# Optimization experiments

Hardware: AMD Instinct MI355X
Metric: run time of the kernel (lower is better)

## Reference

```python
import jax, jax.numpy as jnp
import numpy as np

B, T, C = 2, 2048, 1024
H = 16
D = C // H  # head_dim = 64
EPS = 1e-06
MAX_SEQ = 2048


def make_rotary(dim, max_seq_len, base=10000):
    inv_freq = 1.0 / (base ** (jnp.arange(0, dim, 2, dtype=jnp.float32) / dim))
    pos = jnp.arange(max_seq_len, dtype=jnp.float32)
    sinusoid = jnp.einsum('i,j->ij', pos, inv_freq)  # (S, dim//2)
    return jnp.sin(sinusoid), jnp.cos(sinusoid)


def apply_rotary(x, sin, cos):
    # x: (B, T, H, D); sin/cos: (MAX_SEQ, D//2)
    t = x.shape[1]
    s = sin[:t][:, None, :]  # (T,1,D//2) broadcasts over B and H
    c = cos[:t][:, None, :]
    d = x.shape[-1]
    x1, x2 = x[..., :d // 2], x[..., d // 2:]
    return jnp.concatenate([x1 * c - x2 * s, x2 * c + x1 * s], axis=-1)


def yat_dense(x, kernel, bias, alpha, eps=EPS):
    # Yat layer: squared dot product over squared euclidean distance.
    dot = x @ kernel                                   # (..., out)
    x_sq = jnp.sum(x * x, axis=-1, keepdims=True)      # (..., 1)
    k_sq = jnp.sum(kernel * kernel, axis=0)            # (out,)
    dist = x_sq + k_sq - 2.0 * dot
    y = (dot * dot) / (dist + eps)
    out_f = kernel.shape[1]
    scale = (jnp.sqrt(jnp.float32(out_f)) / jnp.log(1.0 + jnp.float32(out_f))) ** alpha
    return y * scale + bias


def setup_inputs() -> dict:
    key = jax.random.key(0)
    ks = jax.random.split(key, 7)
    x = jax.random.normal(ks[0], (B, T, C), dtype=jnp.float32)
    mask = jnp.tril(jnp.ones((T, T), dtype=bool))[None].repeat(B, axis=0)  # (B,T,T) causal
    s = 1.0 / np.sqrt(C)
    w_attn = jax.random.normal(ks[1], (C, 3 * C), dtype=jnp.float32) * s
    b_attn = jnp.zeros((3 * C,), dtype=jnp.float32)
    a_attn = jnp.ones((1,), dtype=jnp.float32)
    w_proj = jax.random.normal(ks[2], (C, C), dtype=jnp.float32) * s
    b_proj = jnp.zeros((C,), dtype=jnp.float32)
    a_proj = jnp.ones((1,), dtype=jnp.float32)
    return {"x": x, "mask": mask, "w_attn": w_attn, "b_attn": b_attn,
            "a_attn": a_attn, "w_proj": w_proj, "b_proj": b_proj, "a_proj": a_proj}


def reference(x, mask, w_attn, b_attn, a_attn, w_proj, b_proj, a_proj):
    b, t, c = x.shape
    sin, cos = make_rotary(D, MAX_SEQ)
    qkv = yat_dense(x, w_attn, b_attn, a_attn)          # (B,T,3C)
    qkv = qkv.reshape(b, t, 3, H, D)
    q, k, v = jnp.moveaxis(qkv, 2, 0)                   # each (B,T,H,D)
    q = apply_rotary(q, sin, cos)
    k = apply_rotary(k, sin, cos)
    # heads-major layout for attention
    q = q.transpose(0, 2, 1, 3)                          # (B,H,T,D)
    k = k.transpose(0, 2, 1, 3)
    v = v.transpose(0, 2, 1, 3)
    scale = jnp.sqrt(jnp.float32(D))
    attn = jnp.einsum('bhqd,bhkd->bhqk', q, k) / scale   # (B,H,T,T)
    m = mask[:, None, :, :]                              # (B,1,T,T)
    attn = jnp.where(m, attn, jnp.finfo(jnp.float32).min)
    attn = jax.nn.softmax(attn, axis=-1)
    # dropout is identity in deterministic/eval mode
    out = jnp.einsum('bhqk,bhkd->bhqd', attn, v)         # (B,H,T,D)
    out = out.transpose(0, 2, 1, 3).reshape(b, t, c)     # (B,T,C)
    out = yat_dense(out, w_proj, b_proj, a_proj)
    return out
```

## Files before the change

### kernel.cpp

```cpp
#include <hip/hip_runtime.h>
#include <math.h>

#define TSEQ  2048
#define BATCH 2
#define NH    16
#define HD    64
#define CDIM  1024
#define N3C   3072
#define EPSY  1e-6f

typedef unsigned short u16;
typedef unsigned int u32;
typedef __attribute__((ext_vector_type(8))) short bf16x8;
typedef __attribute__((ext_vector_type(4))) float f32x4;

#define MFMA16(a, b, c) __builtin_amdgcn_mfma_f32_16x16x32_bf16(a, b, c, 0, 0, 0)

__device__ __forceinline__ u16 f2bf(float f) {
    unsigned u = __float_as_uint(f);
    return (u16)((u + 0x7fffu + ((u >> 16) & 1u)) >> 16);
}
__device__ __forceinline__ float bf2f(u16 h) {
    return __uint_as_float(((unsigned)h) << 16);
}
__device__ __forceinline__ void gload16(const void* g, void* l) {
    __builtin_amdgcn_global_load_lds(
        (const __attribute__((address_space(1))) unsigned int*)g,
        (__attribute__((address_space(3))) unsigned int*)l, 16, 0, 0);
}

__global__ void rope_init(float2* __restrict__ sc, float* __restrict__ osq) {
    int idx = blockIdx.x * 256 + threadIdx.x;
    if (idx < BATCH * TSEQ) osq[idx] = 0.f;
    int t = idx >> 5, j = idx & 31;
    float inv = exp2f(-(float)j * 0.4152410118609203f);
    float ang = (float)t * inv;
    sc[idx] = make_float2(cosf(ang), sinf(ang));
}

__global__ void colsq_kernel(const float* __restrict__ wa,
                             const float* __restrict__ wp,
                             float* __restrict__ ks) {
    int bid = blockIdx.x, tid = threadIdx.x;
    int c = tid & 63, kq = tid >> 6;
    const float* W; int N, col, outoff;
    if (bid < 48) { W = wa; N = N3C;  col = bid * 64 + c;        outoff = 0;   }
    else          { W = wp; N = CDIM; col = (bid - 48) * 64 + c; outoff = N3C; }
    float s = 0.f;
    int i0 = kq * 256;
    #pragma unroll 4
    for (int i = i0; i < i0 + 256; ++i) {
        float v = W[(size_t)i * N + col];
        s = fmaf(v, v, s);
    }
    __shared__ float red[256];
    red[tid] = s;
    __syncthreads();
    if (kq == 0) ks[outoff + col] = red[c] + red[64 + c] + red[128 + c] + red[192 + c];
}

__global__ void convert_rows(const float* __restrict__ X, u16* __restrict__ Xhi,
                             float* __restrict__ rsq) {
    int row = blockIdx.x, tid = threadIdx.x;
    int lane = tid & 63, wv = tid >> 6;
    size_t base = (size_t)row * CDIM + tid * 4;
    float4 v = *(const float4*)(X + base);
    ushort4 hi;
    hi.x = f2bf(v.x); hi.y = f2bf(v.y); hi.z = f2bf(v.z); hi.w = f2bf(v.w);
    *(ushort4*)(Xhi + base) = hi;
    float s = v.x * v.x + v.y * v.y + v.z * v.z + v.w * v.w;
    #pragma unroll
    for (int off = 32; off; off >>= 1) s += __shfl_down(s, off, 64);
    __shared__ float red[4];
    if (lane == 0) red[wv] = s;
    __syncthreads();
    if (tid == 0) rsq[row] = red[0] + red[1] + red[2] + red[3];
}

__global__ void convert_wT(const float* __restrict__ W, u16* __restrict__ Whi,
                           int K, int N) {
    __shared__ float tile[64][68];
    int k0 = blockIdx.y * 64, n0 = blockIdx.x * 64;
    int tid = threadIdx.x;
    int r = tid >> 4, c4 = (tid & 15) * 4;
    #pragma unroll
    for (int i = 0; i < 4; ++i) {
        int k = k0 + r + i * 16;
        float4 v = *(const float4*)(W + (size_t)k * N + n0 + c4);
        *(float4*)&tile[r + i * 16][c4] = v;
    }
    __syncthreads();
    int n = tid >> 4, k4 = (tid & 15) * 4;
    #pragma unroll
    for (int i = 0; i < 4; ++i) {
        int nn = n + i * 16;
        ushort4 hi;
        hi.x = f2bf(tile[k4 + 0][nn]);
        hi.y = f2bf(tile[k4 + 1][nn]);
        hi.z = f2bf(tile[k4 + 2][nn]);
        hi.w = f2bf(tile[k4 + 3][nn]);
        *(ushort4*)(Whi + (size_t)(n0 + nn) * K + k0 + k4) = hi;
    }
}

__global__ __launch_bounds__(256, 4) void gemm1_fused(
    const u16* __restrict__ Ah, const u16* __restrict__ Bh,
    const float* __restrict__ bias, const float* __restrict__ rowsq,
    const float* __restrict__ colsq, const float* __restrict__ alphap,
    const float2* __restrict__ ropeSC,
    u16* __restrict__ Qb, u16* __restrict__ Kb, u16* __restrict__ Vt) {
    constexpr int BK = 32;
    const int K = CDIM;
    __shared__ u16 Ash[128 * BK], Bsh[128 * BK];
    int tid = threadIdx.x;
    int lane = tid & 63, wv = tid >> 6;
    int quad = lane >> 4, l15 = lane & 15;
    int wr = wv >> 1, wc = wv & 1;
    int bm = blockIdx.y * 128, bn = blockIdx.x * 128;
    int rsub = lane >> 2;
    int lc8 = (lane & 3) * 8;
    int gc8 = (((lane & 3) - (rsub >> 1)) & 3) * 8;
    int pf8 = ((quad + (l15 >> 1)) & 3) * 8;

    f32x4 acc[4][4];
    #pragma unroll
    for (int i = 0; i < 4; ++i)
        #pragma unroll
        for (int j = 0; j < 4; ++j) acc[i][j] = (f32x4){0.f, 0.f, 0.f, 0.f};

    for (int kt = 0; kt < K; kt += BK) {
        #pragma unroll
        for (int i = 0; i < 2; ++i) {
            int r = i * 64 + wv * 16 + rsub;
            gload16(Ah + (size_t)(bm + r) * K + kt + gc8, &Ash[r * BK + lc8]);
            gload16(Bh + (size_t)(bn + r) * K + kt + gc8, &Bsh[r * BK + lc8]);
        }
        __syncthreads();
        bf16x8 fah[4], fbh[4];
        #pragma unroll
        for (int i = 0; i < 4; ++i)
            fah[i] = *(const bf16x8*)&Ash[(wr * 64 + i * 16 + l15) * BK + pf8];
        #pragma unroll
        for (int j = 0; j < 4; ++j)
            fbh[j] = *(const bf16x8*)&Bsh[(wc * 64 + j * 16 + l15) * BK + pf8];
        #pragma unroll
        for (int i = 0; i < 4; ++i)
            #pragma unroll
            for (int j = 0; j < 4; ++j)
                acc[i][j] = MFMA16(fah[i], fbh[j], acc[i][j]);
        __syncthreads();
    }

    float alpha = alphap[0];
    float scale = powf(sqrtf((float)N3C) / logf(1.0f + (float)N3C), alpha);
    int segc0 = bn + wc * 64;
    int seg = segc0 >> 10;
    int h = (segc0 >> 6) & 15;
    int bglob = bm >> 11;
    int bh = bglob * NH + h;

    if (seg < 2) {
        u16* dst = (seg == 0) ? Qb : Kb;
        float qs = (seg == 0) ? 0.125f : 1.0f;
        #pragma unroll
        for (int i = 0; i < 4; ++i) {
            int tb = bm + wr * 64 + i * 16 + quad * 4;
            #pragma unroll
            for (int r = 0; r < 4; ++r) {
                int row = tb + r;
                int t = row & (TSEQ - 1);
                float rs = rowsq[row];
                float y[4];
                #pragma unroll
                for (int j = 0; j < 4; ++j) {
                    int col = segc0 + j * 16 + l15;
                    float dot = acc[i][j][r];
                    float dist = rs + colsq[col] - 2.0f * dot + EPSY;
                    y[j] = dot * dot / dist * scale + bias[col];
                }
                float2 sc0 = ropeSC[t * 32 + l15];
                float2 sc1 = ropeSC[t * 32 + 16 + l15];
                float c0 = sc0.x, s0 = sc0.y, c1 = sc1.x, s1 = sc1.y;
                size_t ob = ((size_t)bh * TSEQ + t) * HD;
                dst[ob + l15]      = f2bf((y[0] * c0 - y[2] * s0) * qs);
                dst[ob + 16 + l15] = f2bf((y[1] * c1 - y[3] * s1) * qs);
                dst[ob + 32 + l15] = f2bf((y[2] * c0 + y[0] * s0) * qs);
                dst[ob + 48 + l15] = f2bf((y[3] * c1 + y[1] * s1) * qs);
            }
        }
    } else {
        #pragma unroll
        for (int i = 0; i < 4; ++i) {
            int tb = bm + wr * 64 + i * 16 + quad * 4;
            int t0 = tb & (TSEQ - 1);
            #pragma unroll
            for (int j = 0; j < 4; ++j) {
                int col = segc0 + j * 16 + l15;
                int d = j * 16 + l15;
                float cs = colsq[col], bi = bias[col];
                ushort4 pk;
                u16* pp = (u16*)&pk;
                #pragma unroll
                for (int r = 0; r < 4; ++r) {
                    float dot = acc[i][j][r];
                    float dist = rowsq[tb + r] + cs - 2.0f * dot + EPSY;
                    pp[r] = f2bf(dot * dot / dist * scale + bi);
                }
                *(ushort4*)(Vt + ((size_t)bh * HD + d) * TSEQ + t0) = pk;
            }
        }
    }
}

__global__ __launch_bounds__(256, 4) void gemm_yat_mfma(
    const u16* __restrict__ Ah, const u16* __restrict__ Bh,
    const float* __restrict__ bias, const float* __restrict__ rowsq,
    const float* __restrict__ colsq, const float* __restrict__ alphap,
    float* __restrict__ outp, int M, int N, int K, float outf) {
    constexpr int BM = 128, BN = 64, BK = 32;
    __shared__ u16 Ash[BM * BK], Bsh[BN * BK];
    int tid = threadIdx.x;
    int lane = tid & 63, wv = tid >> 6;
    int quad = lane >> 4, l15 = lane & 15;
    int bm = blockIdx.y * BM, bn = blockIdx.x * BN;
    int rsub = lane >> 2;
    int lc8 = (lane & 3) * 8;
    int gc8 = (((lane & 3) - (rsub >> 1)) & 3) * 8;
    int pf8 = ((quad + (l15 >> 1)) & 3) * 8;

    f32x4 acc[2][4];
    #pragma unroll
    for (int i = 0; i < 2; ++i)
        #pragma unroll
        for (int j = 0; j < 4; ++j) acc[i][j] = (f32x4){0.f, 0.f, 0.f, 0.f};

    for (int kt = 0; kt < K; kt += BK) {
        #pragma unroll
        for (int i = 0; i < 2; ++i) {
            int r = i * 64 + wv * 16 + rsub;
            gload16(Ah + (size_t)(bm + r) * K + kt + gc8, &Ash[r * BK + lc8]);
        }
        {
            int r = wv * 16 + rsub;
            gload16(Bh + (size_t)(bn + r) * K + kt + gc8, &Bsh[r * BK + lc8]);
        }
        __syncthreads();
        bf16x8 fah[2], fbh[4];
        #pragma unroll
        for (int i = 0; i < 2; ++i)
            fah[i] = *(const bf16x8*)&Ash[(wv * 32 + i * 16 + l15) * BK + pf8];
        #pragma unroll
        for (int j = 0; j < 4; ++j)
            fbh[j] = *(const bf16x8*)&Bsh[(j * 16 + l15) * BK + pf8];
        #pragma unroll
        for (int i = 0; i < 2; ++i)
            #pragma unroll
            for (int j = 0; j < 4; ++j)
                acc[i][j] = MFMA16(fah[i], fbh[j], acc[i][j]);
        __syncthreads();
    }

    float alpha = alphap[0];
    float scale = powf(sqrtf(outf) / logf(1.0f + outf), alpha);
    #pragma unroll
    for (int j = 0; j < 4; ++j) {
        int col = bn + j * 16 + l15;
        float cs = colsq[col], bi = bias[col];
        #pragma unroll
        for (int i = 0; i < 2; ++i) {
            #pragma unroll
            for (int r = 0; r < 4; ++r) {
                int row = bm + wv * 32 + i * 16 + quad * 4 + r;
                float dot = acc[i][j][r];
                float dist = rowsq[row] + cs - 2.0f * dot + EPSY;
                outp[(size_t)row * N + col] = dot * dot / dist * scale + bi;
            }
        }
    }
}

__global__ __launch_bounds__(256) void attn_mfma(
    const u16* __restrict__ Qb, const u16* __restrict__ Kb,
    const u16* __restrict__ Vt, u16* __restrict__ Chi,
    float* __restrict__ osq) {
    __shared__ u16 Ksh[64 * 64];
    __shared__ u16 Vsh[64 * 64];
    int tid = threadIdx.x;
    int lane = tid & 63, wv = tid >> 6;
    int quad = lane >> 4, l15 = lane & 15;
    int bh = blockIdx.x;
    int b = bh >> 4, h = bh & 15;
    const u16* Qh = Qb + (size_t)bh * TSEQ * HD;
    const u16* Kh = Kb + (size_t)bh * TSEQ * HD;
    const u16* Vh = Vt + (size_t)bh * HD * TSEQ;
    const f32x4 zf = {0.f, 0.f, 0.f, 0.f};

    int qb = 31 - blockIdx.y;
    int qw = qb * 64 + wv * 16;
    bf16x8 bq0 = *(const bf16x8*)(Qh + (size_t)(qw + l15) * HD + quad * 8);
    bf16x8 bq1 = *(const bf16x8*)(Qh + (size_t)(qw + l15) * HD + 32 + quad * 8);

    f32x4 o[4] = {zf, zf, zf, zf};
    float l = 0.f;

    for (int kt = 0; kt <= qb; ++kt) {
        int k0 = kt * 64;
        __syncthreads();
        #pragma unroll
        for (int p = 0; p < 2; ++p) {
            int lin = p * 256 + tid;
            int rowi = lin >> 3, ch = lin & 7;
            int gk = (ch + rowi) & 7;
            gload16(Kh + (size_t)(k0 + rowi) * HD + gk * 8, &Ksh[lin * 8]);
            gload16(Vh + (size_t)rowi * TSEQ + k0 + gk * 8, &Vsh[lin * 8]);
        }
        __syncthreads();

        f32x4 st[4];
        #pragma unroll
        for (int mt = 0; mt < 4; ++mt) {
            int key = mt * 16 + l15;
            bf16x8 a0 = *(const bf16x8*)&Ksh[key * 64 + ((quad - key) & 7) * 8];
            bf16x8 a1 = *(const bf16x8*)&Ksh[key * 64 + ((4 + quad - key) & 7) * 8];
            st[mt] = MFMA16(a0, bq0, zf);
            st[mt] = MFMA16(a1, bq1, st[mt]);
        }
        if (kt == qb) {
            int q = qw + l15;
            #pragma unroll
            for (int mt = 0; mt < 4; ++mt)
                #pragma unroll
                for (int r = 0; r < 4; ++r)
                    if (k0 + mt * 16 + quad * 4 + r > q) st[mt][r] = -1e30f;
        }
        u32 pp[4][2];
        #pragma unroll
        for (int mt = 0; mt < 4; ++mt) {
            float p0 = __expf(st[mt][0]);
            float p1 = __expf(st[mt][1]);
            float p2 = __expf(st[mt][2]);
            float p3 = __expf(st[mt][3]);
            l += (p0 + p1) + (p2 + p3);
            pp[mt][0] = (u32)f2bf(p0) | ((u32)f2bf(p1) << 16);
            pp[mt][1] = (u32)f2bf(p2) | ((u32)f2bf(p3) << 16);
        }
        #pragma unroll
        for (int s = 0; s < 2; ++s) {
            u32 bw[4];
            #pragma unroll
            for (int w = 0; w < 4; ++w) {
                int srcl = (((quad & 1) * 2 + (w >> 1)) << 4) + l15;
                u32 vlo = (u32)__shfl((int)pp[2 * s][w & 1], srcl, 64);
                u32 vhi = (u32)__shfl((int)pp[2 * s + 1][w & 1], srcl, 64);
                bw[w] = (quad & 2) ? vhi : vlo;
            }
            bf16x8 bfr;
            *(u32*)&((short*)&bfr)[0] = bw[0];
            *(u32*)&((short*)&bfr)[2] = bw[1];
            *(u32*)&((short*)&bfr)[4] = bw[2];
            *(u32*)&((short*)&bfr)[6] = bw[3];
            #pragma unroll
            for (int dt = 0; dt < 4; ++dt) {
                int d = dt * 16 + l15;
                bf16x8 av = *(const bf16x8*)&Vsh[d * 64 + ((s * 4 + quad - d) & 7) * 8];
                o[dt] = MFMA16(av, bfr, o[dt]);
            }
        }
    }

    l += __shfl_xor(l, 16, 64);
    l += __shfl_xor(l, 32, 64);
    float inv = 1.0f / l;
    int row = (b << 11) + qw + l15;
    float ss = 0.f;
    #pragma unroll
    for (int dt = 0; dt < 4; ++dt) {
        float v0 = o[dt][0] * inv, v1 = o[dt][1] * inv;
        float v2 = o[dt][2] * inv, v3 = o[dt][3] * inv;
        ss += v0 * v0 + v1 * v1 + v2 * v2 + v3 * v3;
        ushort4 pk;
        pk.x = f2bf(v0); pk.y = f2bf(v1); pk.z = f2bf(v2); pk.w = f2bf(v3);
        *(ushort4*)(Chi + (size_t)row * CDIM + h * HD + dt * 16 + quad * 4) = pk;
    }
    ss += __shfl_xor(ss, 16, 64);
    ss += __shfl_xor(ss, 32, 64);
    if (quad == 0) atomicAdd(osq + row, ss);
}

extern "C" void kernel_launch(void* const* d_in, const int* in_sizes, int n_in,
                              void* d_out, int out_size, void* d_ws, size_t ws_size,
                              hipStream_t stream) {
    const float* x      = (const float*)d_in[0];
    const float* w_attn = (const float*)d_in[2];
    const float* b_attn = (const float*)d_in[3];
    const float* a_attn = (const float*)d_in[4];
    const float* w_proj = (const float*)d_in[5];
    const float* b_proj = (const float*)d_in[6];
    const float* a_proj = (const float*)d_in[7];
    float* outp = (float*)d_out;

    char* ws = (char*)d_ws;
    float* ksq = (float*)(ws);
    float* xsq = (float*)(ws + 16384);
    float* osq = (float*)(ws + 32768);
    char* pA  = ws + 65536;
    u16* Ahi = (u16*)pA;
    u16* Chi = (u16*)pA;
    char* pWt = pA + 16777216;
    u16* Wthi = (u16*)pWt;
    char* pWp = pWt + 6291456;
    u16* Wphi = (u16*)pWp;
    char* pQ = pWp + 2097152;
    u16* Qb = (u16*)pQ;
    u16* Kb = (u16*)(pQ + 8388608);
    u16* Vt = (u16*)(pQ + 16777216);
    float2* ropeSC = (float2*)(pQ + 25165824);

    rope_init<<<256, 256, 0, stream>>>(ropeSC, osq);
    colsq_kernel<<<64, 256, 0, stream>>>(w_attn, w_proj, ksq);
    convert_rows<<<BATCH * TSEQ, 256, 0, stream>>>(x, Ahi, xsq);
    convert_wT<<<dim3(N3C / 64, CDIM / 64), 256, 0, stream>>>(w_attn, Wthi, CDIM, N3C);
    convert_wT<<<dim3(CDIM / 64, CDIM / 64), 256, 0, stream>>>(w_proj, Wphi, CDIM, CDIM);
    gemm1_fused<<<dim3(N3C / 128, (BATCH * TSEQ) / 128), 256, 0, stream>>>(
        Ahi, Wthi, b_attn, xsq, ksq, a_attn, ropeSC, Qb, Kb, Vt);
    attn_mfma<<<dim3(BATCH * NH, 32), 256, 0, stream>>>(Qb, Kb, Vt, Chi, osq);
    gemm_yat_mfma<<<dim3(CDIM / 64, (BATCH * TSEQ) / 128), 256, 0, stream>>>(
        Chi, Wphi, b_proj, osq, ksq + N3C, a_proj, outp,
        BATCH * TSEQ, CDIM, CDIM, (float)CDIM);
}
```

Before: 248.8 us.

## Merge prep kernels into one launch and split attention blocks into half-size query tiles

Five preprocessing kernels (rope table, column norms, row conversion, two weight transposes) are merged into a single launch that dispatches on block index, removing four launch gaps. The attention kernel now uses 128-thread blocks covering 32 queries instead of 256 threads covering 64, doubling the grid so more blocks can be spread across CUs. The cost is that each K/V tile is loaded twice as often in total. The diagonal masking logic must still match the finer query split.

```diff
diff --git a/kernel.cpp b/kernel.cpp
--- a/kernel.cpp
+++ b/kernel.cpp
@@ -29,77 +29,81 @@
         (__attribute__((address_space(3))) unsigned int*)l, 16, 0, 0);
 }
 
-__global__ void rope_init(float2* __restrict__ sc, float* __restrict__ osq) {
-    int idx = blockIdx.x * 256 + threadIdx.x;
-    if (idx < BATCH * TSEQ) osq[idx] = 0.f;
-    int t = idx >> 5, j = idx & 31;
-    float inv = exp2f(-(float)j * 0.4152410118609203f);
-    float ang = (float)t * inv;
-    sc[idx] = make_float2(cosf(ang), sinf(ang));
-}
-
-__global__ void colsq_kernel(const float* __restrict__ wa,
-                             const float* __restrict__ wp,
-                             float* __restrict__ ks) {
+__global__ __launch_bounds__(256) void prep_kernel(
+    const float* __restrict__ x, const float* __restrict__ wa,
+    const float* __restrict__ wp, u16* __restrict__ Ahi,
+    u16* __restrict__ Wthi, u16* __restrict__ Wphi,
+    float* __restrict__ ksq, float* __restrict__ xsq,
+    float* __restrict__ osq, float2* __restrict__ ropeSC) {
+    __shared__ float smem[64 * 68];
     int bid = blockIdx.x, tid = threadIdx.x;
-    int c = tid & 63, kq = tid >> 6;
-    const float* W; int N, col, outoff;
-    if (bid < 48) { W = wa; N = N3C;  col = bid * 64 + c;        outoff = 0;   }
-    else          { W = wp; N = CDIM; col = (bid - 48) * 64 + c; outoff = N3C; }
-    float s = 0.f;
-    int i0 = kq * 256;
-    #pragma unroll 4
-    for (int i = i0; i < i0 + 256; ++i) {
-        float v = W[(size_t)i * N + col];
-        s = fmaf(v, v, s);
-    }
-    __shared__ float red[256];
-    red[tid] = s;
-    __syncthreads();
-    if (kq == 0) ks[outoff + col] = red[c] + red[64 + c] + red[128 + c] + red[192 + c];
-}
-
-__global__ void convert_rows(const float* __restrict__ X, u16* __restrict__ Xhi,
-                             float* __restrict__ rsq) {
-    int row = blockIdx.x, tid = threadIdx.x;
-    int lane = tid & 63, wv = tid >> 6;
-    size_t base = (size_t)row * CDIM + tid * 4;
-    float4 v = *(const float4*)(X + base);
-    ushort4 hi;
-    hi.x = f2bf(v.x); hi.y = f2bf(v.y); hi.z = f2bf(v.z); hi.w = f2bf(v.w);
-    *(ushort4*)(Xhi + base) = hi;
-    float s = v.x * v.x + v.y * v.y + v.z * v.z + v.w * v.w;
-    #pragma unroll
-    for (int off = 32; off; off >>= 1) s += __shfl_down(s, off, 64);
-    __shared__ float red[4];
-    if (lane == 0) red[wv] = s;
-    __syncthreads();
-    if (tid == 0) rsq[row] = red[0] + red[1] + red[2] + red[3];
-}
-
-__global__ void convert_wT(const float* __restrict__ W, u16* __restrict__ Whi,
-                           int K, int N) {
-    __shared__ float tile[64][68];
-    int k0 = blockIdx.y * 64, n0 = blockIdx.x * 64;
-    int tid = threadIdx.x;
-    int r = tid >> 4, c4 = (tid & 15) * 4;
-    #pragma unroll
-    for (int i = 0; i < 4; ++i) {
-        int k = k0 + r + i * 16;
-        float4 v = *(const float4*)(W + (size_t)k * N + n0 + c4);
-        *(float4*)&tile[r + i * 16][c4] = v;
-    }
-    __syncthreads();
-    int n = tid >> 4, k4 = (tid & 15) * 4;
-    #pragma unroll
-    for (int i = 0; i < 4; ++i) {
-        int nn = n + i * 16;
+
+    if (bid < 4096) {
+        int lane = tid & 63, wv = tid >> 6;
+        size_t base = (size_t)bid * CDIM + tid * 4;
+        float4 v = *(const float4*)(x + base);
         ushort4 hi;
-        hi.x = f2bf(tile[k4 + 0][nn]);
-        hi.y = f2bf(tile[k4 + 1][nn]);
-        hi.z = f2bf(tile[k4 + 2][nn]);
-        hi.w = f2bf(tile[k4 + 3][nn]);
-        *(ushort4*)(Whi + (size_t)(n0 + nn) * K + k0 + k4) = hi;
+        hi.x = f2bf(v.x); hi.y = f2bf(v.y); hi.z = f2bf(v.z); hi.w = f2bf(v.w);
+        *(ushort4*)(Ahi + base) = hi;
+        float s = v.x * v.x + v.y * v.y + v.z * v.z + v.w * v.w;
+        #pragma unroll
+        for (int off = 32; off; off >>= 1) s += __shfl_down(s, off, 64);
+        if (lane == 0) smem[wv] = s;
+        __syncthreads();
+        if (tid == 0) xsq[bid] = smem[0] + smem[1] + smem[2] + smem[3];
+    } else if (bid < 5120) {
+        const float* W; u16* Whi; int K, N, bx, by;
+        if (bid < 4864) {
+            int t = bid - 4096; W = wa; Whi = Wthi; K = CDIM; N = N3C;
+            bx = t % 48; by = t / 48;
+        } else {
+            int t = bid - 4864; W = wp; Whi = Wphi; K = CDIM; N = CDIM;
+            bx = t % 16; by = t / 16;
+        }
+        int k0 = by * 64, n0 = bx * 64;
+        int r = tid >> 4, c4 = (tid & 15) * 4;
+        #pragma unroll
+        for (int i = 0; i < 4; ++i) {
+            int k = k0 + r + i * 16;
+            float4 v = *(const float4*)(W + (size_t)k * N + n0 + c4);
+            *(float4*)&smem[(r + i * 16) * 68 + c4] = v;
+        }
+        __syncthreads();
+        int n = tid >> 4, k4 = (tid & 15) * 4;
+        #pragma unroll
+        for (int i = 0; i < 4; ++i) {
+            int nn = n + i * 16;
+            ushort4 hi;
+            hi.x = f2bf(smem[(k4 + 0) * 68 + nn]);
+            hi.y = f2bf(smem[(k4 + 1) * 68 + nn]);
+            hi.z = f2bf(smem[(k4 + 2) * 68 + nn]);
+            hi.w = f2bf(smem[(k4 + 3) * 68 + nn]);
+            *(ushort4*)(Whi + (size_t)(n0 + nn) * K + k0 + k4) = hi;
+        }
+    } else if (bid < 5184) {
+        int b2 = bid - 5120;
+        int c = tid & 63, kq = tid >> 6;
+        const float* W; int N, col, outoff;
+        if (b2 < 48) { W = wa; N = N3C;  col = b2 * 64 + c;        outoff = 0;   }
+        else         { W = wp; N = CDIM; col = (b2 - 48) * 64 + c; outoff = N3C; }
+        float s = 0.f;
+        int i0 = kq * 256;
+        #pragma unroll 4
+        for (int i = i0; i < i0 + 256; ++i) {
+            float v = W[(size_t)i * N + col];
+            s = fmaf(v, v, s);
+        }
+        smem[tid] = s;
+        __syncthreads();
+        if (kq == 0)
+            ksq[outoff + col] = smem[c] + smem[64 + c] + smem[128 + c] + smem[192 + c];
+    } else {
+        int idx = (bid - 5184) * 256 + tid;
+        if (idx < BATCH * TSEQ) osq[idx] = 0.f;
+        int t = idx >> 5, j = idx & 31;
+        float inv = exp2f(-(float)j * 0.4152410118609203f);
+        float ang = (float)t * inv;
+        ropeSC[idx] = make_float2(cosf(ang), sinf(ang));
     }
 }
 
@@ -279,7 +283,7 @@
     }
 }
 
-__global__ __launch_bounds__(256) void attn_mfma(
+__global__ __launch_bounds__(128) void attn_mfma(
     const u16* __restrict__ Qb, const u16* __restrict__ Kb,
     const u16* __restrict__ Vt, u16* __restrict__ Chi,
     float* __restrict__ osq) {
@@ -295,8 +299,9 @@
     const u16* Vh = Vt + (size_t)bh * HD * TSEQ;
     const f32x4 zf = {0.f, 0.f, 0.f, 0.f};
 
-    int qb = 31 - blockIdx.y;
-    int qw = qb * 64 + wv * 16;
+    int qb = 31 - (blockIdx.y >> 1);
+    int half = blockIdx.y & 1;
+    int qw = qb * 64 + half * 32 + wv * 16;
     bf16x8 bq0 = *(const bf16x8*)(Qh + (size_t)(qw + l15) * HD + quad * 8);
     bf16x8 bq1 = *(const bf16x8*)(Qh + (size_t)(qw + l15) * HD + 32 + quad * 8);
 
@@ -307,8 +312,8 @@
         int k0 = kt * 64;
         __syncthreads();
         #pragma unroll
-        for (int p = 0; p < 2; ++p) {
-            int lin = p * 256 + tid;
+        for (int p = 0; p < 4; ++p) {
+            int lin = p * 128 + tid;
             int rowi = lin >> 3, ch = lin & 7;
             int gk = (ch + rowi) & 7;
             gload16(Kh + (size_t)(k0 + rowi) * HD + gk * 8, &Ksh[lin * 8]);
@@ -416,14 +421,11 @@
     u16* Vt = (u16*)(pQ + 16777216);
     float2* ropeSC = (float2*)(pQ + 25165824);
 
-    rope_init<<<256, 256, 0, stream>>>(ropeSC, osq);
-    colsq_kernel<<<64, 256, 0, stream>>>(w_attn, w_proj, ksq);
-    convert_rows<<<BATCH * TSEQ, 256, 0, stream>>>(x, Ahi, xsq);
-    convert_wT<<<dim3(N3C / 64, CDIM / 64), 256, 0, stream>>>(w_attn, Wthi, CDIM, N3C);
-    convert_wT<<<dim3(CDIM / 64, CDIM / 64), 256, 0, stream>>>(w_proj, Wphi, CDIM, CDIM);
+    prep_kernel<<<5440, 256, 0, stream>>>(
+        x, w_attn, w_proj, Ahi, Wthi, Wphi, ksq, xsq, osq, ropeSC);
     gemm1_fused<<<dim3(N3C / 128, (BATCH * TSEQ) / 128), 256, 0, stream>>>(
         Ahi, Wthi, b_attn, xsq, ksq, a_attn, ropeSC, Qb, Kb, Vt);
-    attn_mfma<<<dim3(BATCH * NH, 32), 256, 0, stream>>>(Qb, Kb, Vt, Chi, osq);
+    attn_mfma<<<dim3(BATCH * NH, 64), 128, 0, stream>>>(Qb, Kb, Vt, Chi, osq);
     gemm_yat_mfma<<<dim3(CDIM / 64, (BATCH * TSEQ) / 128), 256, 0, stream>>>(
         Chi, Wphi, b_proj, osq, ksq + N3C, a_proj, outp,
         BATCH * TSEQ, CDIM, CDIM, (float)CDIM);
```

Result: faster. 241.1 us (-3.1%).
